# Optimization experiments

Measured on AMD Instinct MI355X. Metric: run time of the kernel, lower is better.

## Reference

```python
import jax, jax.numpy as jnp
import numpy as np

# Dimensions
B = 8192      # batch
IN = 1024     # input_dim = feature_count(64) * embedding_dim(16)
D = 8         # domain_count
S = 4         # shared_expert_num
E = 2         # domain_expert_num
H1, H2 = 512, 256   # expert_units
G = 64        # gate hidden
NE = S + D * E      # 20 stacked experts


def setup_inputs() -> dict:
    key = jax.random.key(0)
    ks = jax.random.split(key, 16)
    sd = 0.02
    inp = {
        "x": jax.random.normal(ks[0], (B, IN), jnp.float32),
        "domain_ids": jax.random.randint(ks[1], (B,), 0, D, dtype=jnp.int64),
        # all expert MLPs stacked: first S are shared, next D*E are domain experts (domain-major)
        "eW1": jax.random.normal(ks[2], (NE, IN, H1), jnp.float32) * sd,
        "eb1": jnp.zeros((NE, H1), jnp.float32),
        "eW2": jax.random.normal(ks[3], (NE, H1, H2), jnp.float32) * sd,
        "eb2": jnp.zeros((NE, H2), jnp.float32),
        # per-domain PLE gates: MLP IN -> G -> (S+E), softmax
        "gW1": jax.random.normal(ks[4], (D, IN, G), jnp.float32) * sd,
        "gb1": jnp.zeros((D, G), jnp.float32),
        "gW2": jax.random.normal(ks[5], (D, G, S + E), jnp.float32) * sd,
        "gb2": jnp.zeros((D, S + E), jnp.float32),
        # ExplicitLabelSpace gate: MLP IN -> G -> D, softmax
        "lW1": jax.random.normal(ks[6], (IN, G), jnp.float32) * sd,
        "lb1": jnp.zeros((G,), jnp.float32),
        "lW2": jax.random.normal(ks[7], (G, D), jnp.float32) * sd,
        "lb2": jnp.zeros((D,), jnp.float32),
        # per-domain towers Linear(H2, 1)
        "tW": jax.random.normal(ks[8], (D, H2), jnp.float32) * sd,
        "tb": jnp.zeros((D,), jnp.float32),
    }
    return inp


def reference(x, domain_ids, eW1, eb1, eW2, eb2, gW1, gb1, gW2, gb2,
              lW1, lb1, lW2, lb2, tW, tb):
    # ---- all expert MLPs in two batched GEMMs (ReLU hidden + ReLU final) ----
    h1 = jax.nn.relu(jnp.einsum('bi,eih->beh', x, eW1) + eb1)          # [B,NE,H1]
    h2 = jax.nn.relu(jnp.einsum('beh,eho->beo', h1, eW2) + eb2)        # [B,NE,H2]
    shared = h2[:, :S]                                                  # [B,S,F]
    dom = h2[:, S:].reshape(x.shape[0], D, E, H2).transpose(1, 0, 2, 3) # [D,B,E,F]

    # ---- per-domain gates over concat(shared, domain) experts ----
    gh = jax.nn.relu(jnp.einsum('bi,dig->dbg', x, gW1) + gb1[:, None, :])
    gates = jax.nn.softmax(jnp.einsum('dbg,dgo->dbo', gh, gW2) + gb2[:, None, :], axis=-1)  # [D,B,S+E]
    g_s, g_d = gates[..., :S], gates[..., S:]
    # weighted sum of concatenated experts, without materializing the broadcast concat
    dres = (jnp.einsum('bsf,dbs->dbf', shared, g_s)
            + jnp.einsum('dbef,dbe->dbf', dom, g_d))                    # [D,B,F]

    # ---- ExplicitLabelSpace: detach all domains except each sample's own ----
    lg = jax.nn.softmax(jax.nn.relu(x @ lW1 + lb1) @ lW2 + lb2, axis=-1)  # [B,D]
    det = jax.lax.stop_gradient(dres)
    own = (jnp.arange(D)[:, None] == domain_ids[None, :])[:, :, None]     # [D,B,1]
    mixed = jnp.where(own, dres, det)                                     # [D,B,F]
    hmoe_out = jnp.einsum('bd,dbf->bf', lg, mixed)                        # [B,F]

    # ---- domain towers (masked per-domain Linear -> one gathered GEMV) ----
    logits = jnp.sum(hmoe_out * tW[domain_ids], axis=-1) + tb[domain_ids]  # [B]
    return jax.nn.sigmoid(logits)
```

## Files before the change

### kernel.cpp

```cpp
#include <hip/hip_runtime.h>
#include <hip/hip_bf16.h>

typedef __hip_bfloat16 bf16;
typedef __attribute__((ext_vector_type(8))) short short8;
typedef __attribute__((ext_vector_type(4))) float f32x4;

#define DEVINL __device__ __forceinline__

DEVINL void gload_lds16(const void* g, void* lds) {
  __builtin_amdgcn_global_load_lds(
      (const __attribute__((address_space(1))) unsigned int*)g,
      (__attribute__((address_space(3))) unsigned int*)lds,
      16, 0, 0);
}


__global__ void k_convert_bf16(const float* __restrict__ in, bf16* __restrict__ out, int n) {
  int i = (blockIdx.x * blockDim.x + threadIdx.x) * 4;
  if (i + 3 < n) {
    float4 v = *(const float4*)(in + i);
    out[i + 0] = __float2bfloat16(v.x);
    out[i + 1] = __float2bfloat16(v.y);
    out[i + 2] = __float2bfloat16(v.z);
    out[i + 3] = __float2bfloat16(v.w);
  }
}

__global__ void k_transpose_to_bf16(const float* __restrict__ in, bf16* __restrict__ out,
                                    int R, int C, long long in_bstride, long long out_bstride) {
  __shared__ float tile[32][33];
  in  += (long long)blockIdx.z * in_bstride;
  out += (long long)blockIdx.z * out_bstride;
  int c0 = blockIdx.x * 32, r0 = blockIdx.y * 32;
  int tx = threadIdx.x, ty = threadIdx.y;
  #pragma unroll
  for (int i = ty; i < 32; i += 8)
    tile[i][tx] = in[(long long)(r0 + i) * C + c0 + tx];
  __syncthreads();
  #pragma unroll
  for (int i = ty; i < 32; i += 8)
    out[(long long)(c0 + i) * R + r0 + tx] = __float2bfloat16(tile[tx][i]);
}

__global__ void k_pack_misc(const float* __restrict__ gb1, const float* __restrict__ lb1,
                            float* __restrict__ gbias, bf16* __restrict__ Wgt) {
  int i = blockIdx.x * blockDim.x + threadIdx.x;
  if (i < 640) {
    float v;
    if (i < 512) v = gb1[i];
    else if (i < 576) v = lb1[i - 512];
    else v = 0.f;
    gbias[i] = v;
  }
  if (i < 64 * 1024) Wgt[576 * 1024 + i] = __float2bfloat16(0.f);
}

template <bool RELU>
__global__ __launch_bounds__(256, 2) void k_gemm_bt(
    const bf16* __restrict__ A, long long a_bstride, int lda,
    const bf16* __restrict__ Bt, long long b_bstride,
    const float* __restrict__ bias, long long bias_bstride,
    bf16* __restrict__ C, long long c_bstride,
    int N, int K) {
  __shared__ __align__(16) short sA[128 * 64];
  __shared__ __align__(16) short sB[128 * 64];

  const int tid = threadIdx.x;
  const int wave = tid >> 6, lane = tid & 63;
  const int e = blockIdx.z;
  const int m0 = blockIdx.y * 128, n0 = blockIdx.x * 128;

  A    += (long long)e * a_bstride;
  Bt   += (long long)e * b_bstride;
  bias += (long long)e * bias_bstride;
  C    += (long long)e * c_bstride;

  const int wm = (wave >> 1) * 64, wn = (wave & 1) * 64;

  f32x4 acc[4][4];
  #pragma unroll
  for (int m = 0; m < 4; ++m)
    #pragma unroll
    for (int n = 0; n < 4; ++n)
      acc[m][n] = (f32x4){0.f, 0.f, 0.f, 0.f};

  const int KT = K >> 6;
  for (int kt = 0; kt < KT; ++kt) {
    const int k0 = kt << 6;
    #pragma unroll
    for (int c = 0; c < 4; ++c) {
      int i = c * 256 + tid;
      int r = i >> 3, col = (i & 7) * 8;
      gload_lds16(A + (size_t)(m0 + r) * lda + k0 + col,
                  (char*)sA + (c * 256 + wave * 64) * 16);
    }
    #pragma unroll
    for (int c = 0; c < 4; ++c) {
      int i = c * 256 + tid;
      int r = i >> 3, col = (i & 7) * 8;
      gload_lds16(Bt + (size_t)(n0 + r) * K + k0 + col,
                  (char*)sB + (c * 256 + wave * 64) * 16);
    }
    __syncthreads();

    #pragma unroll
    for (int ks = 0; ks < 2; ++ks) {
      const int kb = ks * 32 + (lane >> 4) * 8;
      short8 af[4], bfr[4];
      #pragma unroll
      for (int m = 0; m < 4; ++m)
        af[m] = *(const short8*)&sA[(wm + m * 16 + (lane & 15)) * 64 + kb];
      #pragma unroll
      for (int n = 0; n < 4; ++n)
        bfr[n] = *(const short8*)&sB[(wn + n * 16 + (lane & 15)) * 64 + kb];
      #pragma unroll
      for (int m = 0; m < 4; ++m)
        #pragma unroll
        for (int n = 0; n < 4; ++n)
          acc[m][n] = __builtin_amdgcn_mfma_f32_16x16x32_bf16(af[m], bfr[n], acc[m][n], 0, 0, 0);
    }
    __syncthreads();
  }

  #pragma unroll
  for (int m = 0; m < 4; ++m) {
    #pragma unroll
    for (int n = 0; n < 4; ++n) {
      #pragma unroll
      for (int j = 0; j < 4; ++j) {
        int row = m0 + wm + m * 16 + (lane >> 4) * 4 + j;
        int col = n0 + wn + n * 16 + (lane & 15);
        float v = acc[m][n][j] + bias[col];
        if (RELU) v = fmaxf(v, 0.f);
        C[(size_t)row * N + col] = __float2bfloat16(v);
      }
    }
  }
}

__global__ __launch_bounds__(256, 2) void k_gemm2_fused(
    const bf16* __restrict__ A, long long a_bstride, int lda,
    const bf16* __restrict__ Bt, long long b_bstride,
    const float* __restrict__ bias, long long bias_bstride,
    const float* __restrict__ tW, const int* __restrict__ dom_ids,
    float* __restrict__ sPart, int e_base, int K) {
  __shared__ __align__(16) short sA[128 * 64];
  __shared__ __align__(16) short sB[128 * 64];
  __shared__ float sTW[8][128];
  __shared__ int   sdom[128];
  __shared__ float sRed[128];

  const int tid = threadIdx.x;
  const int wave = tid >> 6, lane = tid & 63;
  const int e = blockIdx.z;
  const int m0 = blockIdx.y * 128, n0 = blockIdx.x * 128;

  A    += (long long)e * a_bstride;
  Bt   += (long long)e * b_bstride;
  bias += (long long)e * bias_bstride;

  for (int i = tid; i < 8 * 128; i += 256)
    sTW[i >> 7][i & 127] = tW[(i >> 7) * 256 + n0 + (i & 127)];
  if (tid < 128) sdom[tid] = dom_ids[m0 + tid];

  const int wm = (wave >> 1) * 64, wn = (wave & 1) * 64;

  f32x4 acc[4][4];
  #pragma unroll
  for (int m = 0; m < 4; ++m)
    #pragma unroll
    for (int n = 0; n < 4; ++n)
      acc[m][n] = (f32x4){0.f, 0.f, 0.f, 0.f};

  const int KT = K >> 6;
  for (int kt = 0; kt < KT; ++kt) {
    const int k0 = kt << 6;
    #pragma unroll
    for (int c = 0; c < 4; ++c) {
      int i = c * 256 + tid;
      int r = i >> 3, col = (i & 7) * 8;
      gload_lds16(A + (size_t)(m0 + r) * lda + k0 + col,
                  (char*)sA + (c * 256 + wave * 64) * 16);
    }
    #pragma unroll
    for (int c = 0; c < 4; ++c) {
      int i = c * 256 + tid;
      int r = i >> 3, col = (i & 7) * 8;
      gload_lds16(Bt + (size_t)(n0 + r) * K + k0 + col,
                  (char*)sB + (c * 256 + wave * 64) * 16);
    }
    __syncthreads();

    #pragma unroll
    for (int ks = 0; ks < 2; ++ks) {
      const int kb = ks * 32 + (lane >> 4) * 8;
      short8 af[4], bfr[4];
      #pragma unroll
      for (int m = 0; m < 4; ++m)
        af[m] = *(const short8*)&sA[(wm + m * 16 + (lane & 15)) * 64 + kb];
      #pragma unroll
      for (int n = 0; n < 4; ++n)
        bfr[n] = *(const short8*)&sB[(wn + n * 16 + (lane & 15)) * 64 + kb];
      #pragma unroll
      for (int m = 0; m < 4; ++m)
        #pragma unroll
        for (int n = 0; n < 4; ++n)
          acc[m][n] = __builtin_amdgcn_mfma_f32_16x16x32_bf16(af[m], bfr[n], acc[m][n], 0, 0, 0);
    }
    __syncthreads();
  }

  float rowsum[4][4];
  #pragma unroll
  for (int m = 0; m < 4; ++m) {
    #pragma unroll
    for (int j = 0; j < 4; ++j) {
      int rl = wm + m * 16 + (lane >> 4) * 4 + j;
      int dm = sdom[rl];
      float rs = 0.f;
      #pragma unroll
      for (int n = 0; n < 4; ++n) {
        int cl = wn + n * 16 + (lane & 15);
        float v = fmaxf(acc[m][n][j] + bias[n0 + cl], 0.f);
        rs += v * sTW[dm][cl];
      }
      rowsum[m][j] = rs;
    }
  }
  #pragma unroll
  for (int m = 0; m < 4; ++m)
    #pragma unroll
    for (int j = 0; j < 4; ++j) {
      float v = rowsum[m][j];
      #pragma unroll
      for (int off = 1; off < 16; off <<= 1)
        v += __shfl_xor(v, off);
      rowsum[m][j] = v;
    }
  if ((wave & 1) == 0 && (lane & 15) == 0) {
    #pragma unroll
    for (int m = 0; m < 4; ++m)
      #pragma unroll
      for (int j = 0; j < 4; ++j)
        sRed[wm + m * 16 + (lane >> 4) * 4 + j] = rowsum[m][j];
  }
  __syncthreads();
  if ((wave & 1) == 1 && (lane & 15) == 0) {
    #pragma unroll
    for (int m = 0; m < 4; ++m)
      #pragma unroll
      for (int j = 0; j < 4; ++j)
        sRed[wm + m * 16 + (lane >> 4) * 4 + j] += rowsum[m][j];
  }
  __syncthreads();
  if (tid < 128)
    sPart[((size_t)blockIdx.x * 20 + e_base + e) * 8192 + m0 + tid] = sRed[tid];
}

__global__ void k_gating2(const bf16* __restrict__ gh,
                          const float* __restrict__ gW2, const float* __restrict__ gb2,
                          const float* __restrict__ lW2, const float* __restrict__ lb2,
                          float* __restrict__ wout) {
  const int b = blockIdx.x, lane = threadIdx.x;
  __shared__ float sg[576];
  __shared__ float spre[56];
  __shared__ float sgate[48];
  __shared__ float slg[8];
  const bf16* row = gh + (long long)b * 640;
  for (int i = lane; i < 576; i += 64) sg[i] = __bfloat162float(row[i]);
  __syncthreads();
  if (lane < 48) {
    int d = lane / 6, o = lane % 6;
    float acc = gb2[d * 6 + o];
    const float* w = gW2 + (d * 64) * 6 + o;
    #pragma unroll 8
    for (int g = 0; g < 64; ++g) acc += sg[d * 64 + g] * w[g * 6];
    spre[lane] = acc;
  } else if (lane < 56) {
    int dd = lane - 48;
    float acc = lb2[dd];
    #pragma unroll 8
    for (int g = 0; g < 64; ++g) acc += sg[512 + g] * lW2[g * 8 + dd];
    spre[lane] = acc;
  }
  __syncthreads();
  if (lane < 8) {
    float mx = -1e30f;
    #pragma unroll
    for (int o = 0; o < 6; ++o) mx = fmaxf(mx, spre[lane * 6 + o]);
    float s = 0.f, ev[6];
    #pragma unroll
    for (int o = 0; o < 6; ++o) { ev[o] = expf(spre[lane * 6 + o] - mx); s += ev[o]; }
    float inv = 1.f / s;
    #pragma unroll
    for (int o = 0; o < 6; ++o) sgate[lane * 6 + o] = ev[o] * inv;
  } else if (lane == 8) {
    float mx = -1e30f;
    #pragma unroll
    for (int d = 0; d < 8; ++d) mx = fmaxf(mx, spre[48 + d]);
    float s = 0.f, ev[8];
    #pragma unroll
    for (int d = 0; d < 8; ++d) { ev[d] = expf(spre[48 + d] - mx); s += ev[d]; }
    float inv = 1.f / s;
    #pragma unroll
    for (int d = 0; d < 8; ++d) slg[d] = ev[d] * inv;
  }
  __syncthreads();
  if (lane < 20) {
    float wv;
    if (lane < 4) {
      wv = 0.f;
      #pragma unroll
      for (int d = 0; d < 8; ++d) wv += slg[d] * sgate[d * 6 + lane];
    } else {
      int idx = lane - 4, d = idx >> 1, ei = idx & 1;
      wv = slg[d] * sgate[d * 6 + 4 + ei];
    }
    wout[(long long)b * 20 + lane] = wv;
  }
}

__global__ void k_final2(const float* __restrict__ sPart, const float* __restrict__ wgt,
                         const int* __restrict__ dom_ids, const float* __restrict__ tb,
                         float* __restrict__ out) {
  int b = blockIdx.x * 256 + threadIdx.x;
  int dom = dom_ids[b];
  float acc = tb[dom];
  const float* w = wgt + (size_t)b * 20;
  #pragma unroll
  for (int e = 0; e < 20; ++e)
    acc += w[e] * (sPart[(size_t)e * 8192 + b] + sPart[(size_t)(20 + e) * 8192 + b]);
  out[b] = 1.f / (1.f + expf(-acc));
}


extern "C" void kernel_launch(void* const* d_in, const int* in_sizes, int n_in,
                              void* d_out, int out_size, void* d_ws, size_t ws_size,
                              hipStream_t stream) {
  const float* x   = (const float*)d_in[0];
  const int*   dom = (const int*)d_in[1];
  const float* eW1 = (const float*)d_in[2];
  const float* eb1 = (const float*)d_in[3];
  const float* eW2 = (const float*)d_in[4];
  const float* eb2 = (const float*)d_in[5];
  const float* gW1 = (const float*)d_in[6];
  const float* gb1 = (const float*)d_in[7];
  const float* gW2 = (const float*)d_in[8];
  const float* gb2 = (const float*)d_in[9];
  const float* lW1 = (const float*)d_in[10];
  const float* lb1 = (const float*)d_in[11];
  const float* lW2 = (const float*)d_in[12];
  const float* lb2 = (const float*)d_in[13];
  const float* tW  = (const float*)d_in[14];
  const float* tb  = (const float*)d_in[15];
  float* out = (float*)d_out;

  char* ws = (char*)d_ws;
  size_t off = 0;
  auto alloc = [&](size_t bytes) -> char* {
    char* p = ws + off;
    off += (bytes + 255) / 256 * 256;
    return p;
  };
  bf16*  xb    = (bf16*) alloc((size_t)8192 * 1024 * 2);
  bf16*  eW1t  = (bf16*) alloc((size_t)20 * 512 * 1024 * 2);
  bf16*  eW2t  = (bf16*) alloc((size_t)20 * 256 * 512 * 2);
  bf16*  Wgt   = (bf16*) alloc((size_t)640 * 1024 * 2);
  float* gbias = (float*)alloc(640 * 4);
  bf16*  gh    = (bf16*) alloc((size_t)8192 * 640 * 2);
  float* wgt   = (float*)alloc((size_t)8192 * 20 * 4);
  float* sPart = (float*)alloc((size_t)2 * 20 * 8192 * 4);
  const size_t per_e = (size_t)8192 * 512 * 2;
  int G = 20;
  {
    size_t avail = (ws_size > off) ? (ws_size - off) : 0;
    size_t g = avail / per_e;
    if (g < 1) g = 1;
    if (g > 20) g = 20;
    G = (int)g;
  }
  bf16* h1 = (bf16*)alloc(per_e * G);

  k_convert_bf16<<<8192, 256, 0, stream>>>(x, xb, 8192 * 1024);
  k_transpose_to_bf16<<<dim3(16, 32, 20), dim3(32, 8), 0, stream>>>(
      eW1, eW1t, 1024, 512, 1024LL * 512, 512LL * 1024);
  k_transpose_to_bf16<<<dim3(8, 16, 20), dim3(32, 8), 0, stream>>>(
      eW2, eW2t, 512, 256, 512LL * 256, 256LL * 512);
  k_transpose_to_bf16<<<dim3(2, 32, 8), dim3(32, 8), 0, stream>>>(
      gW1, Wgt, 1024, 64, 1024LL * 64, 64LL * 1024);
  k_transpose_to_bf16<<<dim3(2, 32, 1), dim3(32, 8), 0, stream>>>(
      lW1, Wgt + 512 * 1024, 1024, 64, 0, 0);
  k_pack_misc<<<256, 256, 0, stream>>>(gb1, lb1, gbias, Wgt);

  k_gemm_bt<true><<<dim3(5, 64, 1), 256, 0, stream>>>(
      xb, 0, 1024, Wgt, 0, gbias, 0, gh, 0, 640, 1024);
  k_gating2<<<8192, 64, 0, stream>>>(gh, gW2, gb2, lW2, lb2, wgt);

  for (int base = 0; base < 20; base += G) {
    int Gc = (20 - base < G) ? (20 - base) : G;
    k_gemm_bt<true><<<dim3(4, 64, Gc), 256, 0, stream>>>(
        xb, 0, 1024, eW1t + (size_t)base * 512 * 1024, 512LL * 1024,
        eb1 + base * 512, 512, h1, 8192LL * 512, 512, 1024);
    k_gemm2_fused<<<dim3(2, 64, Gc), 256, 0, stream>>>(
        h1, 8192LL * 512, 512, eW2t + (size_t)base * 256 * 512, 256LL * 512,
        eb2 + base * 256, 256, tW, dom, sPart, base, 512);
  }

  k_final2<<<32, 256, 0, stream>>>(sPart, wgt, dom, tb, out);
}
```

Measured before the change: 489.5 us.

## Widen fused second GEMM to full-N tiles and add XCD-aware block swizzle

The fused second-layer GEMM now runs 512-thread blocks that each cover all 256 output columns for a 128-row tile. The A tile (h1) is loaded once instead of twice, and the two partial tower dot-products and their extra sPart buffer are no longer needed. Both GEMM kernels remap block ids so that consecutive tiles land on the same XCD, which is meant to improve L2 reuse of shared weights and inputs. The cost is higher LDS use per block (about 56KB) and hardcoded dimensions, which may reduce occupancy.

Result: slower. 502.3 us (+2.6%).

```diff
diff --git a/kernel.cpp b/kernel.cpp
--- a/kernel.cpp
+++ b/kernel.cpp
@@ -12,6 +12,11 @@
       (const __attribute__((address_space(1))) unsigned int*)g,
       (__attribute__((address_space(3))) unsigned int*)lds,
       16, 0, 0);
+}
+
+DEVINL int xcd_swizzle(int fid, int nwg) {
+  if (nwg & 7) return fid;
+  return (fid & 7) * (nwg >> 3) + (fid >> 3);
 }
 
 
@@ -67,8 +72,14 @@
 
   const int tid = threadIdx.x;
   const int wave = tid >> 6, lane = tid & 63;
-  const int e = blockIdx.z;
-  const int m0 = blockIdx.y * 128, n0 = blockIdx.x * 128;
+
+  const int nwg = gridDim.x * gridDim.y * gridDim.z;
+  int fid = blockIdx.x + gridDim.x * (blockIdx.y + gridDim.y * blockIdx.z);
+  int nid = xcd_swizzle(fid, nwg);
+  const int bx = nid % gridDim.x;  nid /= gridDim.x;
+  const int by = nid % gridDim.y;
+  const int e  = nid / gridDim.y;
+  const int m0 = by * 128, n0 = bx * 128;
 
   A    += (long long)e * a_bstride;
   Bt   += (long long)e * b_bstride;
@@ -138,32 +149,36 @@
   }
 }
 
-__global__ __launch_bounds__(256, 2) void k_gemm2_fused(
-    const bf16* __restrict__ A, long long a_bstride, int lda,
-    const bf16* __restrict__ Bt, long long b_bstride,
-    const float* __restrict__ bias, long long bias_bstride,
+__global__ __launch_bounds__(512, 2) void k_gemm2_fused(
+    const bf16* __restrict__ A,
+    const bf16* __restrict__ Bt,
+    const float* __restrict__ bias,
     const float* __restrict__ tW, const int* __restrict__ dom_ids,
-    float* __restrict__ sPart, int e_base, int K) {
+    float* __restrict__ sPart, int e_base) {
   __shared__ __align__(16) short sA[128 * 64];
-  __shared__ __align__(16) short sB[128 * 64];
-  __shared__ float sTW[8][128];
+  __shared__ __align__(16) short sB[256 * 64];
+  __shared__ float sTW[8][256];
   __shared__ int   sdom[128];
-  __shared__ float sRed[128];
+  __shared__ float sRed[4][128];
 
   const int tid = threadIdx.x;
   const int wave = tid >> 6, lane = tid & 63;
-  const int e = blockIdx.z;
-  const int m0 = blockIdx.y * 128, n0 = blockIdx.x * 128;
-
-  A    += (long long)e * a_bstride;
-  Bt   += (long long)e * b_bstride;
-  bias += (long long)e * bias_bstride;
-
-  for (int i = tid; i < 8 * 128; i += 256)
-    sTW[i >> 7][i & 127] = tW[(i >> 7) * 256 + n0 + (i & 127)];
+
+  const int nwg = gridDim.x * gridDim.y;
+  int fid = blockIdx.x + gridDim.x * blockIdx.y;
+  int nid = xcd_swizzle(fid, nwg);
+  const int m0 = (nid % 64) * 128;
+  const int e  = nid / 64;
+
+  A    += (size_t)e * (8192LL * 512);
+  Bt   += (size_t)e * (256LL * 512);
+  bias += e * 256;
+
+  for (int i = tid; i < 8 * 256; i += 512)
+    sTW[i >> 8][i & 255] = tW[i];
   if (tid < 128) sdom[tid] = dom_ids[m0 + tid];
 
-  const int wm = (wave >> 1) * 64, wn = (wave & 1) * 64;
+  const int wm = (wave & 1) * 64, wn = (wave >> 1) * 64;
 
   f32x4 acc[4][4];
   #pragma unroll
@@ -172,22 +187,21 @@
     for (int n = 0; n < 4; ++n)
       acc[m][n] = (f32x4){0.f, 0.f, 0.f, 0.f};
 
-  const int KT = K >> 6;
-  for (int kt = 0; kt < KT; ++kt) {
+  for (int kt = 0; kt < 8; ++kt) {
     const int k0 = kt << 6;
     #pragma unroll
+    for (int c = 0; c < 2; ++c) {
+      int i = c * 512 + tid;
+      int r = i >> 3, col = (i & 7) * 8;
+      gload_lds16(A + (size_t)(m0 + r) * 512 + k0 + col,
+                  (char*)sA + (c * 512 + wave * 64) * 16);
+    }
+    #pragma unroll
     for (int c = 0; c < 4; ++c) {
-      int i = c * 256 + tid;
+      int i = c * 512 + tid;
       int r = i >> 3, col = (i & 7) * 8;
-      gload_lds16(A + (size_t)(m0 + r) * lda + k0 + col,
-                  (char*)sA + (c * 256 + wave * 64) * 16);
-    }
-    #pragma unroll
-    for (int c = 0; c < 4; ++c) {
-      int i = c * 256 + tid;
-      int r = i >> 3, col = (i & 7) * 8;
-      gload_lds16(Bt + (size_t)(n0 + r) * K + k0 + col,
-                  (char*)sB + (c * 256 + wave * 64) * 16);
+      gload_lds16(Bt + (size_t)r * 512 + k0 + col,
+                  (char*)sB + (c * 512 + wave * 64) * 16);
     }
     __syncthreads();
 
@@ -221,7 +235,7 @@
       #pragma unroll
       for (int n = 0; n < 4; ++n) {
         int cl = wn + n * 16 + (lane & 15);
-        float v = fmaxf(acc[m][n][j] + bias[n0 + cl], 0.f);
+        float v = fmaxf(acc[m][n][j] + bias[cl], 0.f);
         rs += v * sTW[dm][cl];
       }
       rowsum[m][j] = rs;
@@ -237,24 +251,19 @@
         v += __shfl_xor(v, off);
       rowsum[m][j] = v;
     }
-  if ((wave & 1) == 0 && (lane & 15) == 0) {
+  const int ncol = wave >> 1;
+  if ((lane & 15) == 0) {
     #pragma unroll
     for (int m = 0; m < 4; ++m)
       #pragma unroll
       for (int j = 0; j < 4; ++j)
-        sRed[wm + m * 16 + (lane >> 4) * 4 + j] = rowsum[m][j];
+        sRed[ncol][wm + m * 16 + (lane >> 4) * 4 + j] = rowsum[m][j];
   }
   __syncthreads();
-  if ((wave & 1) == 1 && (lane & 15) == 0) {
-    #pragma unroll
-    for (int m = 0; m < 4; ++m)
-      #pragma unroll
-      for (int j = 0; j < 4; ++j)
-        sRed[wm + m * 16 + (lane >> 4) * 4 + j] += rowsum[m][j];
-  }
-  __syncthreads();
-  if (tid < 128)
-    sPart[((size_t)blockIdx.x * 20 + e_base + e) * 8192 + m0 + tid] = sRed[tid];
+  if (tid < 128) {
+    float v = sRed[0][tid] + sRed[1][tid] + sRed[2][tid] + sRed[3][tid];
+    sPart[(size_t)(e_base + e) * 8192 + m0 + tid] = v;
+  }
 }
 
 __global__ void k_gating2(const bf16* __restrict__ gh,
@@ -329,7 +338,7 @@
   const float* w = wgt + (size_t)b * 20;
   #pragma unroll
   for (int e = 0; e < 20; ++e)
-    acc += w[e] * (sPart[(size_t)e * 8192 + b] + sPart[(size_t)(20 + e) * 8192 + b]);
+    acc += w[e] * sPart[(size_t)e * 8192 + b];
   out[b] = 1.f / (1.f + expf(-acc));
 }
 
@@ -369,7 +378,7 @@
   float* gbias = (float*)alloc(640 * 4);
   bf16*  gh    = (bf16*) alloc((size_t)8192 * 640 * 2);
   float* wgt   = (float*)alloc((size_t)8192 * 20 * 4);
-  float* sPart = (float*)alloc((size_t)2 * 20 * 8192 * 4);
+  float* sPart = (float*)alloc((size_t)20 * 8192 * 4);
   const size_t per_e = (size_t)8192 * 512 * 2;
   int G = 20;
   {
@@ -401,9 +410,9 @@
     k_gemm_bt<true><<<dim3(4, 64, Gc), 256, 0, stream>>>(
         xb, 0, 1024, eW1t + (size_t)base * 512 * 1024, 512LL * 1024,
         eb1 + base * 512, 512, h1, 8192LL * 512, 512, 1024);
-    k_gemm2_fused<<<dim3(2, 64, Gc), 256, 0, stream>>>(
-        h1, 8192LL * 512, 512, eW2t + (size_t)base * 256 * 512, 256LL * 512,
-        eb2 + base * 256, 256, tW, dom, sPart, base, 512);
+    k_gemm2_fused<<<dim3(64, Gc), 512, 0, stream>>>(
+        h1, eW2t + (size_t)base * 256 * 512,
+        eb2 + base * 256, tW, dom, sPart, base);
   }
 
   k_final2<<<32, 256, 0, stream>>>(sPart, wgt, dom, tb, out);
```
